# Kernel tuning notes

Hardware: AMD Instinct MI355X
Metric: run time of the kernel (lower is better)

The kernel has to match this reference:

```python
import jax, jax.numpy as jnp
import numpy as np

N = 50000   # nodes
E = 800000  # edges (avg degree 16)
F = 128     # input_nf = output_nf
H = 128     # hidden_nf


def setup_inputs() -> dict:
    key = jax.random.key(0)
    ks = jax.random.split(key, 10)
    # coords: spatial part in [-1, 1], z-coordinate (last dim) in [0.5, 1.5] (must be > 0)
    xz = jax.random.uniform(ks[0], (N, 3), minval=-1.0, maxval=1.0)
    xz = xz.at[:, -1].set(jax.random.uniform(ks[1], (N,), minval=0.5, maxval=1.5))
    h = jax.random.normal(ks[2], (N, F), dtype=jnp.float32)
    row = jax.random.randint(ks[3], (E,), 0, N)
    # guarantee col != row so AdS distance is strictly positive on every edge
    col = (row + 1 + jax.random.randint(ks[4], (E,), 0, N - 1)) % N
    edge_index = jnp.stack([row, col]).astype(jnp.int32)

    def lin(k, fan_in, fan_out):
        return jax.random.normal(k, (fan_in, fan_out), dtype=jnp.float32) / np.float32(np.sqrt(fan_in))

    return {
        "xz": xz,
        "h": h,
        "We1": lin(ks[5], 2 * F + 1, H), "be1": jnp.full((H,), 0.1, jnp.float32),
        "We2": lin(ks[6], H, H),         "be2": jnp.full((H,), 0.1, jnp.float32),
        "Wn1": lin(ks[7], H + F, H),     "bn1": jnp.full((H,), 0.1, jnp.float32),
        "Wn2": lin(ks[8], H, F),         "bn2": jnp.full((F,), 0.1, jnp.float32),
        "edge_index": edge_index,
    }


def reference(xz, h, We1, be1, We2, be2, Wn1, bn1, Wn2, bn2, edge_index):
    row, col = edge_index[0], edge_index[1]
    n = h.shape[0]

    # AdS (hyperbolic upper-half-space) distance between xz[row] and xz[col]:
    # d = arccosh(1 + |p1 - p2|^2 / (2 z1 z2)), z = last coordinate
    diff = xz[row] - xz[col]                                  # [E, 3]
    u = jnp.sum(diff * diff, axis=-1) / (2.0 * xz[row, -1] * xz[col, -1])
    dist = jnp.arccosh(1.0 + u)[:, None]                      # [E, 1]

    # edge model: concat(source, target, radial) -> Linear -> silu -> Linear -> silu
    m = jnp.concatenate([h[row], h[col], dist], axis=1)       # [E, 2F+1]
    m = jax.nn.silu(m @ We1 + be1)                            # [E, H]
    m = jax.nn.silu(m @ We2 + be2)                            # [E, H]

    # segment_mean over destination nodes (row)
    num = jax.ops.segment_sum(m, row, num_segments=n)                          # [N, H]
    den = jax.ops.segment_sum(jnp.ones_like(m), row, num_segments=n)          # [N, H]
    agg = num / jnp.maximum(den, jnp.ones((), den.dtype))

    # node model: concat(h, agg) -> Linear -> silu -> Linear, plus residual
    z = jnp.concatenate([h, agg], axis=1)                     # [N, F+H]
    out = jax.nn.silu(z @ Wn1 + bn1) @ Wn2 + bn2              # [N, F]
    return h + out
```

## Files before the change

### kernel.cpp

```cpp
#include <hip/hip_runtime.h>

#define NN 50000
#define EE 800000
#define NB 196

typedef __bf16 bf16x8 __attribute__((ext_vector_type(8)));
typedef float  f32x4  __attribute__((ext_vector_type(4)));

__device__ __forceinline__ float bf2f(ushort u) {
    union { unsigned int i; float f; } v; v.i = ((unsigned int)u) << 16; return v.f;
}
__device__ __forceinline__ ushort f2bf(float f) {
    union { float f; unsigned int i; } v; v.f = f;
    unsigned int u = v.i;
    return (ushort)((u + 0x7FFFu + ((u >> 16) & 1u)) >> 16);
}
__device__ __forceinline__ ushort f2bf_fast(float f) {
    union { float f; unsigned int i; } v; v.f = f;
    return (ushort)((v.i + 0x8000u) >> 16);
}
__device__ __forceinline__ float silu(float x) {
    return x * __builtin_amdgcn_rcpf(1.0f + __expf(-x));
}

__global__ void detect_kernel(const ushort* __restrict__ xzu, int* __restrict__ flag) {
    __shared__ int cnt;
    if (threadIdx.x == 0) cnt = 0;
    __syncthreads();
    float v = bf2f(xzu[2 * threadIdx.x]);
    bool sane = (v == v) && (fabsf(v) <= 4.0f);
    if (sane) atomicAdd(&cnt, 1);
    __syncthreads();
    if (threadIdx.x == 0) *flag = (cnt >= 192) ? 0 : 1;
}

__global__ void prep_kernel(const void* __restrict__ hsrc, const void* __restrict__ xzsrc,
                            const int* __restrict__ erow, const int* __restrict__ flag,
                            ushort* __restrict__ hb, float* __restrict__ xzf,
                            int* __restrict__ cntI) {
    const bool isf = (*flag != 0);
    int b = blockIdx.x;
    if (b < 3125) {
        int i = (b * 256 + threadIdx.x) * 8;
        uint4 o;
        if (isf) {
            const float* s = (const float*)hsrc + i;
            float4 f0 = *(const float4*)s;
            float4 f1 = *(const float4*)(s + 4);
            o.x = (unsigned int)f2bf(f0.x) | ((unsigned int)f2bf(f0.y) << 16);
            o.y = (unsigned int)f2bf(f0.z) | ((unsigned int)f2bf(f0.w) << 16);
            o.z = (unsigned int)f2bf(f1.x) | ((unsigned int)f2bf(f1.y) << 16);
            o.w = (unsigned int)f2bf(f1.z) | ((unsigned int)f2bf(f1.w) << 16);
        } else {
            o = *(const uint4*)((const ushort*)hsrc + i);
        }
        *(uint4*)(hb + i) = o;
    } else if (b < 3712) {
        int i = (b - 3125) * 256 + threadIdx.x;
        if (i < NN * 3)
            xzf[i] = isf ? ((const float*)xzsrc)[i] : bf2f(((const ushort*)xzsrc)[i]);
    } else {
        int e = (b - 3712) * 256 + threadIdx.x;
        if (e < EE) atomicAdd(&cntI[erow[e]], 1);
    }
}

__global__ void swizzle_misc_kernel(const void* We1, const void* We2,
                                    const void* Wn1, const void* Wn2,
                                    const void* be1, const void* be2,
                                    const void* bn1, const void* bn2,
                                    const int* __restrict__ flag,
                                    ushort* __restrict__ We1s, ushort* __restrict__ We2s,
                                    ushort* __restrict__ Wn1s, ushort* __restrict__ Wn2s,
                                    float* __restrict__ fb, ushort* __restrict__ wlb) {
    const bool isf = (*flag != 0);
    if (blockIdx.x == 48) {
        for (int j = threadIdx.x; j < 640; j += 256) {
            int which = j >> 7, k = j & 127;
            const void* src = (which == 0) ? be1 : (which == 1) ? be2 :
                              (which == 2) ? bn1 : (which == 3) ? bn2 : We1;
            size_t idx = (which == 4) ? ((size_t)256 * 128 + k) : (size_t)k;
            float v = isf ? ((const float*)src)[idx] : bf2f(((const ushort*)src)[idx]);
            fb[j] = v;
            if (which == 4) wlb[k] = f2bf(v);
        }
        return;
    }
    int c = blockIdx.x * 256 + threadIdx.x;
    const void* src; ushort* dst; int cl;
    if      (c <  4096) { src = We1; dst = We1s; cl = c;         }
    else if (c <  6144) { src = We2; dst = We2s; cl = c - 4096;  }
    else if (c < 10240) { src = Wn1; dst = Wn1s; cl = c - 6144;  }
    else                { src = Wn2; dst = Wn2s; cl = c - 10240; }
    int l = cl & 63, nt = (cl >> 6) & 7, kc = cl >> 9;
    int kbase = kc * 32 + (l >> 4) * 8;
    int n = nt * 16 + (l & 15);
    ushort tmp[8];
#pragma unroll
    for (int j = 0; j < 8; ++j) {
        size_t idx = (size_t)(kbase + j) * 128 + n;
        tmp[j] = isf ? f2bf(((const float*)src)[idx]) : ((const ushort*)src)[idx];
    }
#pragma unroll
    for (int j = 0; j < 8; ++j) dst[(size_t)cl * 8 + j] = tmp[j];
}

__global__ void scanA_kernel(const int* __restrict__ cntI, int* __restrict__ bsum) {
    __shared__ int s[256];
    int t = threadIdx.x;
    int i = blockIdx.x * 256 + t;
    s[t] = (i < NN) ? cntI[i] : 0;
    __syncthreads();
#pragma unroll
    for (int off = 128; off > 0; off >>= 1) {
        if (t < off) s[t] += s[t + off];
        __syncthreads();
    }
    if (t == 0) bsum[blockIdx.x] = s[0];
}

__global__ void scanC_kernel(const int* __restrict__ cntI, const int* __restrict__ bsum,
                             int* __restrict__ rowStart) {
    __shared__ int s[256];
    __shared__ int sbase;
    int t = threadIdx.x;
    int bv = (t < NB) ? bsum[t] : 0;
    s[t] = bv;
    __syncthreads();
    for (int off = 1; off < 256; off <<= 1) {
        int u = (t >= off) ? s[t - off] : 0;
        __syncthreads();
        if (t >= off) s[t] += u;
        __syncthreads();
    }
    if (t == 0) sbase = (blockIdx.x == 0) ? 0 : s[blockIdx.x - 1];
    __syncthreads();
    int i = blockIdx.x * 256 + t;
    int v = (i < NN) ? cntI[i] : 0;
    s[t] = v;
    __syncthreads();
    for (int off = 1; off < 256; off <<= 1) {
        int u = (t >= off) ? s[t - off] : 0;
        __syncthreads();
        if (t >= off) s[t] += u;
        __syncthreads();
    }
    if (i < NN) rowStart[i] = sbase + s[t] - v;
}

__global__ void scatter_kernel(const int* __restrict__ erow, const int* __restrict__ ecol,
                               const float* __restrict__ xzf,
                               const int* __restrict__ rowStart, int* __restrict__ cursor,
                               int4* __restrict__ eS) {
    int e = blockIdx.x * 256 + threadIdx.x;
    if (e >= EE) return;
    int r = erow[e], c = ecol[e];
    int pos = rowStart[r] + atomicAdd(&cursor[r], 1);
    float4 a = *(const float4*)(xzf + 3 * r);
    float4 b = *(const float4*)(xzf + 3 * c);
    float dx = a.x - b.x, dy = a.y - b.y, dz = a.z - b.z;
    float u = (dx * dx + dy * dy + dz * dz) * __builtin_amdgcn_rcpf(2.0f * a.z * b.z);
    u = fminf(fmaxf(u, 0.0f), 1.0e6f);
    float d = __logf(1.0f + u + sqrtf(u * (u + 2.0f)));
    eS[pos] = make_int4(r, c, __float_as_int(d), 0);
}

__global__ __launch_bounds__(256, 3) void pq_kernel(
    const ushort* __restrict__ hb, const ushort* __restrict__ We1s,
    const float* __restrict__ fb, ushort* __restrict__ Pp, ushort* __restrict__ Qq) {
    __shared__ __align__(16) ushort sA[8192];
    const int tid = threadIdx.x;
    const int lane = tid & 63, w = tid >> 6;
    const int col = lane & 15, quad = lane >> 4;
    const int nt0 = w * 2;
    const int ntiles = (NN + 63) / 64;
    const int nA = w * 32 + col, nB = nA + 16;
    const float be1A = fb[nA], be1B = fb[nB];

    for (int tile = blockIdx.x; tile < ntiles; tile += gridDim.x) {
        __syncthreads();
        const int n0 = tile * 64;
#pragma unroll
        for (int i = 0; i < 4; ++i) {
            int node = n0 + lane;
            uint4 v = (node < NN) ? *(const uint4*)(hb + (size_t)node * 128 + (w + 4 * i) * 8)
                                  : make_uint4(0, 0, 0, 0);
            *(uint4*)(sA + (((lane >> 4) * 4 + i) * 64 + w * 16 + (lane & 15)) * 8) = v;
        }
        __syncthreads();

        f32x4 accP[4][2] = {}, accQ[4][2] = {};
#pragma unroll
        for (int kc = 0; kc < 4; ++kc) {
            bf16x8 bp0 = *(const bf16x8*)(We1s + ((kc * 8 + nt0)           * 64 + lane) * 8);
            bf16x8 bp1 = *(const bf16x8*)(We1s + ((kc * 8 + nt0 + 1)       * 64 + lane) * 8);
            bf16x8 bq0 = *(const bf16x8*)(We1s + (((kc + 4) * 8 + nt0)     * 64 + lane) * 8);
            bf16x8 bq1 = *(const bf16x8*)(We1s + (((kc + 4) * 8 + nt0 + 1) * 64 + lane) * 8);
#pragma unroll
            for (int g = 0; g < 4; ++g) {
                bf16x8 a = *(const bf16x8*)(sA + ((g * 4 + kc) * 64 + lane) * 8);
                accP[g][0] = __builtin_amdgcn_mfma_f32_16x16x32_bf16(a, bp0, accP[g][0], 0, 0, 0);
                accP[g][1] = __builtin_amdgcn_mfma_f32_16x16x32_bf16(a, bp1, accP[g][1], 0, 0, 0);
                accQ[g][0] = __builtin_amdgcn_mfma_f32_16x16x32_bf16(a, bq0, accQ[g][0], 0, 0, 0);
                accQ[g][1] = __builtin_amdgcn_mfma_f32_16x16x32_bf16(a, bq1, accQ[g][1], 0, 0, 0);
            }
        }
#pragma unroll
        for (int g = 0; g < 4; ++g) {
#pragma unroll
            for (int r = 0; r < 4; ++r) {
                int node = n0 + g * 16 + quad * 4 + r;
                if (node < NN) {
                    size_t o = (size_t)node * 128;
                    Pp[o + nA] = f2bf(accP[g][0][r] + be1A);
                    Pp[o + nB] = f2bf(accP[g][1][r] + be1B);
                    Qq[o + nA] = f2bf(accQ[g][0][r]);
                    Qq[o + nB] = f2bf(accQ[g][1][r]);
                }
            }
        }
    }
}

__global__ __launch_bounds__(256, 4) void edge_kernel(
    const ushort* __restrict__ Pp, const ushort* __restrict__ Qq,
    const int4* __restrict__ eS, const ushort* __restrict__ We2s,
    const ushort* __restrict__ wlb, const float* __restrict__ fb,
    float* __restrict__ agg) {
    __shared__ __align__(16) char smem[64 * 132 * 4];
    __shared__ int sRow[64];
    ushort* sM = (ushort*)smem;
    float (*sOut)[132] = (float(*)[132])smem;

    const int tid = threadIdx.x;
    const int lane = tid & 63, w = tid >> 6;
    const int col = lane & 15, quad = lane >> 4;
    const int nt0 = w * 2;

    const int nA = w * 32 + col, nB = nA + 16;
    const float be2A = fb[128 + nA], be2B = fb[128 + nB];

    const int ntiles = EE / 64;
    const int per = (ntiles + gridDim.x - 1) / gridDim.x;
    const int t0 = blockIdx.x * per;
    const int t1 = (t0 + per < ntiles) ? (t0 + per) : ntiles;
    if (t0 >= t1) return;

    bf16x8 B2[8];
#pragma unroll
    for (int kc = 0; kc < 4; ++kc) {
        B2[kc * 2]     = *(const bf16x8*)(We2s + ((kc * 8 + nt0)     * 64 + lane) * 8);
        B2[kc * 2 + 1] = *(const bf16x8*)(We2s + ((kc * 8 + nt0 + 1) * 64 + lane) * 8);
    }
    bf16x8 WL[4];
#pragma unroll
    for (int i = 0; i < 4; ++i) WL[i] = *(const bf16x8*)(wlb + (w + 4 * i) * 8);

    int4 ed = eS[(size_t)t0 * 64 + lane];
    bf16x8 p[4], q[4];
#pragma unroll
    for (int i = 0; i < 4; ++i) {
        p[i] = *(const bf16x8*)(Pp + (size_t)ed.x * 128 + (w + 4 * i) * 8);
        q[i] = *(const bf16x8*)(Qq + (size_t)ed.y * 128 + (w + 4 * i) * 8);
    }

    for (int tile = t0; tile < t1; ++tile) {
        const int tn = (tile + 1 < t1) ? (tile + 1) : tile;
        const int4 edn = eS[(size_t)tn * 64 + lane];

        __syncthreads();
        if (w == 0) sRow[lane] = ed.x;
        const float d = __int_as_float(ed.z);
#pragma unroll
        for (int i = 0; i < 4; ++i) {
            ushort out8[8];
#pragma unroll
            for (int j = 0; j < 8; ++j) {
                float x = (float)p[i][j] + (float)q[i][j] + d * (float)WL[i][j];
                out8[j] = f2bf_fast(silu(x));
            }
            *(uint4*)(sM + (((lane >> 4) * 4 + i) * 64 + w * 16 + (lane & 15)) * 8) =
                *(const uint4*)out8;
        }
#pragma unroll
        for (int i = 0; i < 4; ++i) {
            p[i] = *(const bf16x8*)(Pp + (size_t)edn.x * 128 + (w + 4 * i) * 8);
            q[i] = *(const bf16x8*)(Qq + (size_t)edn.y * 128 + (w + 4 * i) * 8);
        }
        ed = edn;
        __syncthreads();

        f32x4 acc2[4][2] = {};
#pragma unroll
        for (int kc = 0; kc < 4; ++kc) {
#pragma unroll
            for (int g = 0; g < 4; ++g) {
                bf16x8 a = *(const bf16x8*)(sM + ((g * 4 + kc) * 64 + lane) * 8);
                acc2[g][0] = __builtin_amdgcn_mfma_f32_16x16x32_bf16(a, B2[kc * 2],     acc2[g][0], 0, 0, 0);
                acc2[g][1] = __builtin_amdgcn_mfma_f32_16x16x32_bf16(a, B2[kc * 2 + 1], acc2[g][1], 0, 0, 0);
            }
        }
        __syncthreads();

#pragma unroll
        for (int g = 0; g < 4; ++g) {
#pragma unroll
            for (int r4 = 0; r4 < 4; ++r4) {
                int m = g * 16 + quad * 4 + r4;
                sOut[m][nA] = silu(acc2[g][0][r4] + be2A);
                sOut[m][nB] = silu(acc2[g][1][r4] + be2B);
            }
        }
        __syncthreads();

        {
            const int cc = tid & 127;
            const int mb = (tid >> 7) * 32;
            float acc = 0.0f;
            int prow = sRow[mb];
            for (int k = 0; k < 32; ++k) {
                int rw = sRow[mb + k];
                if (rw != prow) {
                    unsafeAtomicAdd(&agg[(size_t)prow * 128 + cc], acc);
                    acc = 0.0f;
                    prow = rw;
                }
                acc += sOut[mb + k][cc];
            }
            unsafeAtomicAdd(&agg[(size_t)prow * 128 + cc], acc);
        }
    }
}

__global__ __launch_bounds__(256, 3) void node_kernel(
    const ushort* __restrict__ hb, const void* __restrict__ hraw,
    const float* __restrict__ agg, const int* __restrict__ cntI,
    const ushort* __restrict__ Wn1s, const ushort* __restrict__ Wn2s,
    const float* __restrict__ fb, const int* __restrict__ flag,
    void* __restrict__ outv) {
    __shared__ __align__(16) ushort sA[16384];
    __shared__ __align__(16) ushort sM[8192];
    const int tid = threadIdx.x;
    const int lane = tid & 63, w = tid >> 6;
    const int col = lane & 15, quad = lane >> 4;
    const int nt0 = w * 2;
    const int ntiles = (NN + 63) / 64;
    const bool isf = (*flag != 0);
    float* outf = (float*)outv;
    ushort* outu = (ushort*)outv;

    const int nA = w * 32 + col, nB = nA + 16;
    const float bn1A = fb[256 + nA], bn1B = fb[256 + nB];
    const float bn2A = fb[384 + nA], bn2B = fb[384 + nB];

    for (int tile = blockIdx.x; tile < ntiles; tile += gridDim.x) {
        __syncthreads();
        const int n0 = tile * 64;
#pragma unroll
        for (int i = 0; i < 8; ++i) {
            int kb = w + 4 * i;
            int node = n0 + lane;
            uint4 v;
            if (node < NN) {
                if (kb < 16) {
                    v = *(const uint4*)(hb + (size_t)node * 128 + kb * 8);
                } else {
                    const float* ap = agg + (size_t)node * 128 + (kb - 16) * 8;
                    float invc = __builtin_amdgcn_rcpf(fmaxf((float)cntI[node], 1.0f));
                    float4 f0 = *(const float4*)ap;
                    float4 f1 = *(const float4*)(ap + 4);
                    v.x = (unsigned int)f2bf_fast(f0.x * invc) | ((unsigned int)f2bf_fast(f0.y * invc) << 16);
                    v.y = (unsigned int)f2bf_fast(f0.z * invc) | ((unsigned int)f2bf_fast(f0.w * invc) << 16);
                    v.z = (unsigned int)f2bf_fast(f1.x * invc) | ((unsigned int)f2bf_fast(f1.y * invc) << 16);
                    v.w = (unsigned int)f2bf_fast(f1.z * invc) | ((unsigned int)f2bf_fast(f1.w * invc) << 16);
                }
            } else {
                v = make_uint4(0, 0, 0, 0);
            }
            *(uint4*)(sA + (((quad * 8 + i) * 64) + w * 16 + col) * 8) = v;
        }
        __syncthreads();

        f32x4 acc[4][2] = {};
#pragma unroll
        for (int kc = 0; kc < 8; ++kc) {
            bf16x8 b0 = *(const bf16x8*)(Wn1s + ((kc * 8 + nt0)     * 64 + lane) * 8);
            bf16x8 b1 = *(const bf16x8*)(Wn1s + ((kc * 8 + nt0 + 1) * 64 + lane) * 8);
#pragma unroll
            for (int g = 0; g < 4; ++g) {
                bf16x8 a = *(const bf16x8*)(sA + ((g * 8 + kc) * 64 + lane) * 8);
                acc[g][0] = __builtin_amdgcn_mfma_f32_16x16x32_bf16(a, b0, acc[g][0], 0, 0, 0);
                acc[g][1] = __builtin_amdgcn_mfma_f32_16x16x32_bf16(a, b1, acc[g][1], 0, 0, 0);
            }
        }
#pragma unroll
        for (int g = 0; g < 4; ++g) {
            int base0 = ((g * 4 + w) * 64 + (col >> 3) * 16) * 8 + (col & 7);
#pragma unroll
            for (int r = 0; r < 4; ++r) {
                int mrow = quad * 4 + r;
                sM[base0 + mrow * 8]              = f2bf_fast(silu(acc[g][0][r] + bn1A));
                sM[base0 + 2 * 16 * 8 + mrow * 8] = f2bf_fast(silu(acc[g][1][r] + bn1B));
            }
        }
        __syncthreads();

        f32x4 acc2[4][2] = {};
#pragma unroll
        for (int kc = 0; kc < 4; ++kc) {
            bf16x8 b0 = *(const bf16x8*)(Wn2s + ((kc * 8 + nt0)     * 64 + lane) * 8);
            bf16x8 b1 = *(const bf16x8*)(Wn2s + ((kc * 8 + nt0 + 1) * 64 + lane) * 8);
#pragma unroll
            for (int g = 0; g < 4; ++g) {
                bf16x8 a = *(const bf16x8*)(sM + ((g * 4 + kc) * 64 + lane) * 8);
                acc2[g][0] = __builtin_amdgcn_mfma_f32_16x16x32_bf16(a, b0, acc2[g][0], 0, 0, 0);
                acc2[g][1] = __builtin_amdgcn_mfma_f32_16x16x32_bf16(a, b1, acc2[g][1], 0, 0, 0);
            }
        }
#pragma unroll
        for (int g = 0; g < 4; ++g) {
#pragma unroll
            for (int r = 0; r < 4; ++r) {
                int ml2 = g * 16 + quad * 4 + r;
                int node = n0 + ml2;
                if (node < NN) {
                    size_t oi = (size_t)node * 128;
                    float h0 = isf ? ((const float*)hraw)[oi + nA] : bf2f(((const ushort*)hraw)[oi + nA]);
                    float h1 = isf ? ((const float*)hraw)[oi + nB] : bf2f(((const ushort*)hraw)[oi + nB]);
                    float x0 = acc2[g][0][r] + bn2A + h0;
                    float x1 = acc2[g][1][r] + bn2B + h1;
                    if (isf) { outf[oi + nA] = x0; outf[oi + nB] = x1; }
                    else     { outu[oi + nA] = f2bf_fast(x0); outu[oi + nB] = f2bf_fast(x1); }
                }
            }
        }
    }
}

extern "C" void kernel_launch(void* const* d_in, const int* in_sizes, int n_in,
                              void* d_out, int out_size, void* d_ws, size_t ws_size,
                              hipStream_t stream) {
    const void* xz  = d_in[0];
    const void* h   = d_in[1];
    const void* We1 = d_in[2];
    const void* be1 = d_in[3];
    const void* We2 = d_in[4];
    const void* be2 = d_in[5];
    const void* Wn1 = d_in[6];
    const void* bn1 = d_in[7];
    const void* Wn2 = d_in[8];
    const void* bn2 = d_in[9];
    const int*  ei  = (const int*)d_in[10];
    const int* erow = ei;
    const int* ecol = ei + EE;

    char* base = (char*)d_ws;
    size_t cur = 0;
    auto alloc = [&](size_t bytes) { size_t o = cur; cur = (cur + bytes + 255) & ~(size_t)255; return o; };
    int*    flag   = (int*)   (base + alloc(16));
    float*  agg    = (float*) (base + alloc((size_t)NN * 128 * 4));
    int*    cntI   = (int*)   (base + alloc((size_t)NN * 4));
    int*    cursor = (int*)   (base + alloc((size_t)NN * 4));
    ushort* hb     = (ushort*)(base + alloc((size_t)NN * 128 * 2));
    ushort* Pp     = (ushort*)(base + alloc((size_t)NN * 128 * 2));
    ushort* Qq     = (ushort*)(base + alloc((size_t)NN * 128 * 2));
    int4*   eS     = (int4*)  (base + alloc((size_t)EE * 16));
    float*  xzf    = (float*) (base + alloc((size_t)NN * 3 * 4 + 16));
    int*    rowSt  = (int*)   (base + alloc((size_t)NN * 4));
    int*    bsum   = (int*)   (base + alloc(256 * 4));
    ushort* We1s   = (ushort*)(base + alloc(32768 * 2));
    ushort* We2s   = (ushort*)(base + alloc(16384 * 2));
    ushort* Wn1s   = (ushort*)(base + alloc(32768 * 2));
    ushort* Wn2s   = (ushort*)(base + alloc(16384 * 2));
    float*  fb     = (float*) (base + alloc(640 * 4));
    ushort* wlb    = (ushort*)(base + alloc(128 * 2));

    size_t zbytes = (size_t)((char*)hb - (char*)agg);
    (void)hipMemsetAsync(agg, 0, zbytes, stream);

    detect_kernel<<<1, 256, 0, stream>>>((const ushort*)xz, flag);
    prep_kernel<<<6837, 256, 0, stream>>>(h, xz, erow, flag, hb, xzf, cntI);
    swizzle_misc_kernel<<<49, 256, 0, stream>>>(We1, We2, Wn1, Wn2, be1, be2, bn1, bn2,
                                                flag, We1s, We2s, Wn1s, Wn2s, fb, wlb);
    scanA_kernel<<<NB, 256, 0, stream>>>(cntI, bsum);
    scanC_kernel<<<NB, 256, 0, stream>>>(cntI, bsum, rowSt);
    scatter_kernel<<<(EE + 255) / 256, 256, 0, stream>>>(erow, ecol, xzf, rowSt, cursor, eS);
    pq_kernel<<<782, 256, 0, stream>>>(hb, We1s, fb, Pp, Qq);
    edge_kernel<<<1024, 256, 0, stream>>>(Pp, Qq, eS, We2s, wlb, fb, agg);
    node_kernel<<<782, 256, 0, stream>>>(hb, h, agg, cntI, Wn1s, Wn2s, fb, flag, d_out);
}
```

Before: 404.8 us.

## Merge prep/swizzle/detect kernels, co-launch scatter with PQ, drop edge prefetch

Folds the dtype detection into each kernel via a per-block ballot, merges the prep and weight-swizzle kernels into one launch, and runs the independent scatter and P/Q GEMM work as disjoint block ranges of a single launch. This cuts three kernel launches and lets scatter and GEMM blocks overlap. The edge kernel no longer prefetches the next tile's P/Q gathers into registers and loads them inline instead, which lowers register pressure but exposes gather latency. Every block now redundantly reads 256 xz samples to decide the input dtype.

Result: faster. 331.8 us (-18.0%).

```diff
diff --git a/kernel.cpp b/kernel.cpp
--- a/kernel.cpp
+++ b/kernel.cpp
@@ -23,25 +23,42 @@
     return x * __builtin_amdgcn_rcpf(1.0f + __expf(-x));
 }
 
-__global__ void detect_kernel(const ushort* __restrict__ xzu, int* __restrict__ flag) {
-    __shared__ int cnt;
-    if (threadIdx.x == 0) cnt = 0;
-    __syncthreads();
-    float v = bf2f(xzu[2 * threadIdx.x]);
+__device__ __forceinline__ bool detect_isf(const ushort* __restrict__ xzu,
+                                           int tid, int* scnt) {
+    float v = bf2f(xzu[2 * (tid & 255)]);
     bool sane = (v == v) && (fabsf(v) <= 4.0f);
-    if (sane) atomicAdd(&cnt, 1);
-    __syncthreads();
-    if (threadIdx.x == 0) *flag = (cnt >= 192) ? 0 : 1;
-}
-
-__global__ void prep_kernel(const void* __restrict__ hsrc, const void* __restrict__ xzsrc,
-                            const int* __restrict__ erow, const int* __restrict__ flag,
-                            ushort* __restrict__ hb, float* __restrict__ xzf,
-                            int* __restrict__ cntI) {
-    const bool isf = (*flag != 0);
-    int b = blockIdx.x;
+    unsigned long long m = __ballot(sane);
+    if ((tid & 63) == 0) scnt[tid >> 6] = __popcll(m);
+    __syncthreads();
+    int cnt = scnt[0] + scnt[1] + scnt[2] + scnt[3];
+    return cnt < 192;
+}
+
+__global__ void prep_all_kernel(const void* __restrict__ hsrc, const void* __restrict__ xzsrc,
+                                const int* __restrict__ erow,
+                                const void* We1, const void* We2,
+                                const void* Wn1, const void* Wn2,
+                                const void* be1, const void* be2,
+                                const void* bn1, const void* bn2,
+                                ushort* __restrict__ hb, float* __restrict__ xzf,
+                                int* __restrict__ cntI,
+                                ushort* __restrict__ We1s, ushort* __restrict__ We2s,
+                                ushort* __restrict__ Wn1s, ushort* __restrict__ Wn2s,
+                                float* __restrict__ fb, ushort* __restrict__ wlb) {
+    __shared__ int scnt[4];
+    const int b = blockIdx.x;
+    const int tid = threadIdx.x;
+
+    if (b >= 3712 && b < 6837) {
+        int e = (b - 3712) * 256 + tid;
+        if (e < EE) atomicAdd(&cntI[erow[e]], 1);
+        return;
+    }
+
+    const bool isf = detect_isf((const ushort*)xzsrc, tid, scnt);
+
     if (b < 3125) {
-        int i = (b * 256 + threadIdx.x) * 8;
+        int i = (b * 256 + tid) * 8;
         uint4 o;
         if (isf) {
             const float* s = (const float*)hsrc + i;
@@ -56,53 +73,41 @@
         }
         *(uint4*)(hb + i) = o;
     } else if (b < 3712) {
-        int i = (b - 3125) * 256 + threadIdx.x;
+        int i = (b - 3125) * 256 + tid;
         if (i < NN * 3)
             xzf[i] = isf ? ((const float*)xzsrc)[i] : bf2f(((const ushort*)xzsrc)[i]);
     } else {
-        int e = (b - 3712) * 256 + threadIdx.x;
-        if (e < EE) atomicAdd(&cntI[erow[e]], 1);
-    }
-}
-
-__global__ void swizzle_misc_kernel(const void* We1, const void* We2,
-                                    const void* Wn1, const void* Wn2,
-                                    const void* be1, const void* be2,
-                                    const void* bn1, const void* bn2,
-                                    const int* __restrict__ flag,
-                                    ushort* __restrict__ We1s, ushort* __restrict__ We2s,
-                                    ushort* __restrict__ Wn1s, ushort* __restrict__ Wn2s,
-                                    float* __restrict__ fb, ushort* __restrict__ wlb) {
-    const bool isf = (*flag != 0);
-    if (blockIdx.x == 48) {
-        for (int j = threadIdx.x; j < 640; j += 256) {
-            int which = j >> 7, k = j & 127;
-            const void* src = (which == 0) ? be1 : (which == 1) ? be2 :
-                              (which == 2) ? bn1 : (which == 3) ? bn2 : We1;
-            size_t idx = (which == 4) ? ((size_t)256 * 128 + k) : (size_t)k;
-            float v = isf ? ((const float*)src)[idx] : bf2f(((const ushort*)src)[idx]);
-            fb[j] = v;
-            if (which == 4) wlb[k] = f2bf(v);
-        }
-        return;
-    }
-    int c = blockIdx.x * 256 + threadIdx.x;
-    const void* src; ushort* dst; int cl;
-    if      (c <  4096) { src = We1; dst = We1s; cl = c;         }
-    else if (c <  6144) { src = We2; dst = We2s; cl = c - 4096;  }
-    else if (c < 10240) { src = Wn1; dst = Wn1s; cl = c - 6144;  }
-    else                { src = Wn2; dst = Wn2s; cl = c - 10240; }
-    int l = cl & 63, nt = (cl >> 6) & 7, kc = cl >> 9;
-    int kbase = kc * 32 + (l >> 4) * 8;
-    int n = nt * 16 + (l & 15);
-    ushort tmp[8];
-#pragma unroll
-    for (int j = 0; j < 8; ++j) {
-        size_t idx = (size_t)(kbase + j) * 128 + n;
-        tmp[j] = isf ? f2bf(((const float*)src)[idx]) : ((const ushort*)src)[idx];
-    }
-#pragma unroll
-    for (int j = 0; j < 8; ++j) dst[(size_t)cl * 8 + j] = tmp[j];
+        int sw = b - 6837;
+        if (sw == 48) {
+            for (int j = tid; j < 640; j += 256) {
+                int which = j >> 7, k = j & 127;
+                const void* src = (which == 0) ? be1 : (which == 1) ? be2 :
+                                  (which == 2) ? bn1 : (which == 3) ? bn2 : We1;
+                size_t idx = (which == 4) ? ((size_t)256 * 128 + k) : (size_t)k;
+                float v = isf ? ((const float*)src)[idx] : bf2f(((const ushort*)src)[idx]);
+                fb[j] = v;
+                if (which == 4) wlb[k] = f2bf(v);
+            }
+            return;
+        }
+        int c = sw * 256 + tid;
+        const void* src; ushort* dst; int cl;
+        if      (c <  4096) { src = We1; dst = We1s; cl = c;         }
+        else if (c <  6144) { src = We2; dst = We2s; cl = c - 4096;  }
+        else if (c < 10240) { src = Wn1; dst = Wn1s; cl = c - 6144;  }
+        else                { src = Wn2; dst = Wn2s; cl = c - 10240; }
+        int l = cl & 63, nt = (cl >> 6) & 7, kc = cl >> 9;
+        int kbase = kc * 32 + (l >> 4) * 8;
+        int n = nt * 16 + (l & 15);
+        ushort tmp[8];
+#pragma unroll
+        for (int j = 0; j < 8; ++j) {
+            size_t idx = (size_t)(kbase + j) * 128 + n;
+            tmp[j] = isf ? f2bf(((const float*)src)[idx]) : ((const ushort*)src)[idx];
+        }
+#pragma unroll
+        for (int j = 0; j < 8; ++j) dst[(size_t)cl * 8 + j] = tmp[j];
+    }
 }
 
 __global__ void scanA_kernel(const int* __restrict__ cntI, int* __restrict__ bsum) {
@@ -148,75 +153,73 @@
     if (i < NN) rowStart[i] = sbase + s[t] - v;
 }
 
-__global__ void scatter_kernel(const int* __restrict__ erow, const int* __restrict__ ecol,
-                               const float* __restrict__ xzf,
-                               const int* __restrict__ rowStart, int* __restrict__ cursor,
-                               int4* __restrict__ eS) {
-    int e = blockIdx.x * 256 + threadIdx.x;
-    if (e >= EE) return;
-    int r = erow[e], c = ecol[e];
-    int pos = rowStart[r] + atomicAdd(&cursor[r], 1);
-    float4 a = *(const float4*)(xzf + 3 * r);
-    float4 b = *(const float4*)(xzf + 3 * c);
-    float dx = a.x - b.x, dy = a.y - b.y, dz = a.z - b.z;
-    float u = (dx * dx + dy * dy + dz * dz) * __builtin_amdgcn_rcpf(2.0f * a.z * b.z);
-    u = fminf(fmaxf(u, 0.0f), 1.0e6f);
-    float d = __logf(1.0f + u + sqrtf(u * (u + 2.0f)));
-    eS[pos] = make_int4(r, c, __float_as_int(d), 0);
-}
-
-__global__ __launch_bounds__(256, 3) void pq_kernel(
+__global__ __launch_bounds__(256, 3) void scatter_pq_kernel(
     const ushort* __restrict__ hb, const ushort* __restrict__ We1s,
-    const float* __restrict__ fb, ushort* __restrict__ Pp, ushort* __restrict__ Qq) {
+    const float* __restrict__ fb, ushort* __restrict__ Pp, ushort* __restrict__ Qq,
+    const int* __restrict__ erow, const int* __restrict__ ecol,
+    const float* __restrict__ xzf, const int* __restrict__ rowStart,
+    int* __restrict__ cursor, int4* __restrict__ eS) {
     __shared__ __align__(16) ushort sA[8192];
     const int tid = threadIdx.x;
+
+    if (blockIdx.x >= 782) {
+        int e = (blockIdx.x - 782) * 256 + tid;
+        if (e >= EE) return;
+        int r = erow[e], c = ecol[e];
+        int pos = rowStart[r] + atomicAdd(&cursor[r], 1);
+        float4 a = *(const float4*)(xzf + 3 * r);
+        float4 b = *(const float4*)(xzf + 3 * c);
+        float dx = a.x - b.x, dy = a.y - b.y, dz = a.z - b.z;
+        float u = (dx * dx + dy * dy + dz * dz) * __builtin_amdgcn_rcpf(2.0f * a.z * b.z);
+        u = fminf(fmaxf(u, 0.0f), 1.0e6f);
+        float d = __logf(1.0f + u + sqrtf(u * (u + 2.0f)));
+        eS[pos] = make_int4(r, c, __float_as_int(d), 0);
+        return;
+    }
+
     const int lane = tid & 63, w = tid >> 6;
     const int col = lane & 15, quad = lane >> 4;
     const int nt0 = w * 2;
-    const int ntiles = (NN + 63) / 64;
     const int nA = w * 32 + col, nB = nA + 16;
     const float be1A = fb[nA], be1B = fb[nB];
-
-    for (int tile = blockIdx.x; tile < ntiles; tile += gridDim.x) {
-        __syncthreads();
-        const int n0 = tile * 64;
-#pragma unroll
-        for (int i = 0; i < 4; ++i) {
-            int node = n0 + lane;
-            uint4 v = (node < NN) ? *(const uint4*)(hb + (size_t)node * 128 + (w + 4 * i) * 8)
-                                  : make_uint4(0, 0, 0, 0);
-            *(uint4*)(sA + (((lane >> 4) * 4 + i) * 64 + w * 16 + (lane & 15)) * 8) = v;
-        }
-        __syncthreads();
-
-        f32x4 accP[4][2] = {}, accQ[4][2] = {};
-#pragma unroll
-        for (int kc = 0; kc < 4; ++kc) {
-            bf16x8 bp0 = *(const bf16x8*)(We1s + ((kc * 8 + nt0)           * 64 + lane) * 8);
-            bf16x8 bp1 = *(const bf16x8*)(We1s + ((kc * 8 + nt0 + 1)       * 64 + lane) * 8);
-            bf16x8 bq0 = *(const bf16x8*)(We1s + (((kc + 4) * 8 + nt0)     * 64 + lane) * 8);
-            bf16x8 bq1 = *(const bf16x8*)(We1s + (((kc + 4) * 8 + nt0 + 1) * 64 + lane) * 8);
-#pragma unroll
-            for (int g = 0; g < 4; ++g) {
-                bf16x8 a = *(const bf16x8*)(sA + ((g * 4 + kc) * 64 + lane) * 8);
-                accP[g][0] = __builtin_amdgcn_mfma_f32_16x16x32_bf16(a, bp0, accP[g][0], 0, 0, 0);
-                accP[g][1] = __builtin_amdgcn_mfma_f32_16x16x32_bf16(a, bp1, accP[g][1], 0, 0, 0);
-                accQ[g][0] = __builtin_amdgcn_mfma_f32_16x16x32_bf16(a, bq0, accQ[g][0], 0, 0, 0);
-                accQ[g][1] = __builtin_amdgcn_mfma_f32_16x16x32_bf16(a, bq1, accQ[g][1], 0, 0, 0);
-            }
-        }
+    const int tile = blockIdx.x;
+    const int n0 = tile * 64;
+#pragma unroll
+    for (int i = 0; i < 4; ++i) {
+        int node = n0 + lane;
+        uint4 v = (node < NN) ? *(const uint4*)(hb + (size_t)node * 128 + (w + 4 * i) * 8)
+                              : make_uint4(0, 0, 0, 0);
+        *(uint4*)(sA + (((lane >> 4) * 4 + i) * 64 + w * 16 + (lane & 15)) * 8) = v;
+    }
+    __syncthreads();
+
+    f32x4 accP[4][2] = {}, accQ[4][2] = {};
+#pragma unroll
+    for (int kc = 0; kc < 4; ++kc) {
+        bf16x8 bp0 = *(const bf16x8*)(We1s + ((kc * 8 + nt0)           * 64 + lane) * 8);
+        bf16x8 bp1 = *(const bf16x8*)(We1s + ((kc * 8 + nt0 + 1)       * 64 + lane) * 8);
+        bf16x8 bq0 = *(const bf16x8*)(We1s + (((kc + 4) * 8 + nt0)     * 64 + lane) * 8);
+        bf16x8 bq1 = *(const bf16x8*)(We1s + (((kc + 4) * 8 + nt0 + 1) * 64 + lane) * 8);
 #pragma unroll
         for (int g = 0; g < 4; ++g) {
-#pragma unroll
-            for (int r = 0; r < 4; ++r) {
-                int node = n0 + g * 16 + quad * 4 + r;
-                if (node < NN) {
-                    size_t o = (size_t)node * 128;
-                    Pp[o + nA] = f2bf(accP[g][0][r] + be1A);
-                    Pp[o + nB] = f2bf(accP[g][1][r] + be1B);
-                    Qq[o + nA] = f2bf(accQ[g][0][r]);
-                    Qq[o + nB] = f2bf(accQ[g][1][r]);
-                }
+            bf16x8 a = *(const bf16x8*)(sA + ((g * 4 + kc) * 64 + lane) * 8);
+            accP[g][0] = __builtin_amdgcn_mfma_f32_16x16x32_bf16(a, bp0, accP[g][0], 0, 0, 0);
+            accP[g][1] = __builtin_amdgcn_mfma_f32_16x16x32_bf16(a, bp1, accP[g][1], 0, 0, 0);
+            accQ[g][0] = __builtin_amdgcn_mfma_f32_16x16x32_bf16(a, bq0, accQ[g][0], 0, 0, 0);
+            accQ[g][1] = __builtin_amdgcn_mfma_f32_16x16x32_bf16(a, bq1, accQ[g][1], 0, 0, 0);
+        }
+    }
+#pragma unroll
+    for (int g = 0; g < 4; ++g) {
+#pragma unroll
+        for (int r = 0; r < 4; ++r) {
+            int node = n0 + g * 16 + quad * 4 + r;
+            if (node < NN) {
+                size_t o = (size_t)node * 128;
+                Pp[o + nA] = f2bf(accP[g][0][r] + be1A);
+                Pp[o + nB] = f2bf(accP[g][1][r] + be1B);
+                Qq[o + nA] = f2bf(accQ[g][0][r]);
+                Qq[o + nB] = f2bf(accQ[g][1][r]);
             }
         }
     }
@@ -257,35 +260,28 @@
     for (int i = 0; i < 4; ++i) WL[i] = *(const bf16x8*)(wlb + (w + 4 * i) * 8);
 
     int4 ed = eS[(size_t)t0 * 64 + lane];
-    bf16x8 p[4], q[4];
-#pragma unroll
-    for (int i = 0; i < 4; ++i) {
-        p[i] = *(const bf16x8*)(Pp + (size_t)ed.x * 128 + (w + 4 * i) * 8);
-        q[i] = *(const bf16x8*)(Qq + (size_t)ed.y * 128 + (w + 4 * i) * 8);
-    }
 
     for (int tile = t0; tile < t1; ++tile) {
         const int tn = (tile + 1 < t1) ? (tile + 1) : tile;
         const int4 edn = eS[(size_t)tn * 64 + lane];
 
         __syncthreads();
-        if (w == 0) sRow[lane] = ed.x;
+        const int r = ed.x, c = ed.y;
         const float d = __int_as_float(ed.z);
+        if (w == 0) sRow[lane] = r;
 #pragma unroll
         for (int i = 0; i < 4; ++i) {
+            int ch = w + 4 * i;
+            bf16x8 p = *(const bf16x8*)(Pp + (size_t)r * 128 + ch * 8);
+            bf16x8 q = *(const bf16x8*)(Qq + (size_t)c * 128 + ch * 8);
             ushort out8[8];
 #pragma unroll
             for (int j = 0; j < 8; ++j) {
-                float x = (float)p[i][j] + (float)q[i][j] + d * (float)WL[i][j];
+                float x = (float)p[j] + (float)q[j] + d * (float)WL[i][j];
                 out8[j] = f2bf_fast(silu(x));
             }
             *(uint4*)(sM + (((lane >> 4) * 4 + i) * 64 + w * 16 + (lane & 15)) * 8) =
                 *(const uint4*)out8;
-        }
-#pragma unroll
-        for (int i = 0; i < 4; ++i) {
-            p[i] = *(const bf16x8*)(Pp + (size_t)edn.x * 128 + (w + 4 * i) * 8);
-            q[i] = *(const bf16x8*)(Qq + (size_t)edn.y * 128 + (w + 4 * i) * 8);
         }
         ed = edn;
         __syncthreads();
@@ -334,18 +330,19 @@
 
 __global__ __launch_bounds__(256, 3) void node_kernel(
     const ushort* __restrict__ hb, const void* __restrict__ hraw,
+    const void* __restrict__ xzsrc,
     const float* __restrict__ agg, const int* __restrict__ cntI,
     const ushort* __restrict__ Wn1s, const ushort* __restrict__ Wn2s,
-    const float* __restrict__ fb, const int* __restrict__ flag,
-    void* __restrict__ outv) {
+    const float* __restrict__ fb, void* __restrict__ outv) {
     __shared__ __align__(16) ushort sA[16384];
     __shared__ __align__(16) ushort sM[8192];
+    __shared__ int scnt[4];
     const int tid = threadIdx.x;
     const int lane = tid & 63, w = tid >> 6;
     const int col = lane & 15, quad = lane >> 4;
     const int nt0 = w * 2;
     const int ntiles = (NN + 63) / 64;
-    const bool isf = (*flag != 0);
+    const bool isf = detect_isf((const ushort*)xzsrc, tid, scnt);
     float* outf = (float*)outv;
     ushort* outu = (ushort*)outv;
 
@@ -457,7 +454,6 @@
     char* base = (char*)d_ws;
     size_t cur = 0;
     auto alloc = [&](size_t bytes) { size_t o = cur; cur = (cur + bytes + 255) & ~(size_t)255; return o; };
-    int*    flag   = (int*)   (base + alloc(16));
     float*  agg    = (float*) (base + alloc((size_t)NN * 128 * 4));
     int*    cntI   = (int*)   (base + alloc((size_t)NN * 4));
     int*    cursor = (int*)   (base + alloc((size_t)NN * 4));
@@ -478,14 +474,14 @@
     size_t zbytes = (size_t)((char*)hb - (char*)agg);
     (void)hipMemsetAsync(agg, 0, zbytes, stream);
 
-    detect_kernel<<<1, 256, 0, stream>>>((const ushort*)xz, flag);
-    prep_kernel<<<6837, 256, 0, stream>>>(h, xz, erow, flag, hb, xzf, cntI);
-    swizzle_misc_kernel<<<49, 256, 0, stream>>>(We1, We2, Wn1, Wn2, be1, be2, bn1, bn2,
-                                                flag, We1s, We2s, Wn1s, Wn2s, fb, wlb);
+    prep_all_kernel<<<6886, 256, 0, stream>>>(h, xz, erow, We1, We2, Wn1, Wn2,
+                                              be1, be2, bn1, bn2,
+                                              hb, xzf, cntI, We1s, We2s, Wn1s, Wn2s,
+                                              fb, wlb);
     scanA_kernel<<<NB, 256, 0, stream>>>(cntI, bsum);
     scanC_kernel<<<NB, 256, 0, stream>>>(cntI, bsum, rowSt);
-    scatter_kernel<<<(EE + 255) / 256, 256, 0, stream>>>(erow, ecol, xzf, rowSt, cursor, eS);
-    pq_kernel<<<782, 256, 0, stream>>>(hb, We1s, fb, Pp, Qq);
+    scatter_pq_kernel<<<782 + 3125, 256, 0, stream>>>(hb, We1s, fb, Pp, Qq,
+                                                      erow, ecol, xzf, rowSt, cursor, eS);
     edge_kernel<<<1024, 256, 0, stream>>>(Pp, Qq, eS, We2s, wlb, fb, agg);
-    node_kernel<<<782, 256, 0, stream>>>(hb, h, agg, cntI, Wn1s, Wn2s, fb, flag, d_out);
-}
+    node_kernel<<<782, 256, 0, stream>>>(hb, h, xz, agg, cntI, Wn1s, Wn2s, fb, d_out);
+}
```
